# Performance work log

Hardware: AMD Instinct MI355X
Metric: run time of the kernel (lower is better)

## Reference

```python
import jax, jax.numpy as jnp
import numpy as np

B, C, H, W = 8, 384, 32, 32
HEADS = 12


def _relative_position_index(h, w):
    coords_h = np.arange(h)
    coords_w = np.arange(w)
    coords = np.stack(np.meshgrid(coords_h, coords_w, indexing='ij'))  # [2,h,w]
    flat = coords.reshape(2, -1)  # [2, N]
    rel = flat[:, :, None] - flat[:, None, :]  # [2, N, N]
    rel = rel.transpose(1, 2, 0)  # [N, N, 2]
    rel[:, :, 0] += h - 1
    rel[:, :, 1] += w - 1
    rel[:, :, 0] *= 2 * w - 1
    return rel.sum(-1).astype(np.int32)  # [N, N]


def setup_inputs() -> dict:
    key = jax.random.key(0)
    ks = jax.random.split(key, 6)
    std = 0.02
    x = jax.random.normal(ks[0], (B, C, H, W), dtype=jnp.float32)
    q_w = jax.random.normal(ks[1], (C, C), dtype=jnp.float32) * std
    q_b = jnp.zeros((C,), dtype=jnp.float32)
    kv_w = jax.random.normal(ks[2], (2 * C, C), dtype=jnp.float32) * std
    kv_b = jnp.zeros((2 * C,), dtype=jnp.float32)
    proj_w = jax.random.normal(ks[3], (C, C), dtype=jnp.float32) * std
    proj_b = jnp.zeros((C,), dtype=jnp.float32)
    n_table = (2 * H - 1) * (2 * W - 1)
    rpb_table = jax.random.normal(ks[4], (n_table, HEADS), dtype=jnp.float32) * std
    rel_index = jnp.asarray(_relative_position_index(H, W))  # [N, N] int32
    return {"x": x, "q_w": q_w, "q_b": q_b, "kv_w": kv_w, "kv_b": kv_b,
            "proj_w": proj_w, "proj_b": proj_b, "rpb_table": rpb_table,
            "rel_index": rel_index}


def reference(x, q_w, q_b, kv_w, kv_b, proj_w, proj_b, rpb_table, rel_index):
    b, c, h, w = x.shape
    n = h * w
    heads = rpb_table.shape[-1]
    hd = c // heads
    scale = hd ** (-0.5)

    xf = x.reshape(b, c, n)  # 1x1 conv == per-pixel matmul
    q = jnp.einsum('dc,bcn->bdn', q_w, xf) + q_b[:, None]
    q = q.reshape(b, heads, hd, n).transpose(0, 1, 3, 2)  # [b,h,n,hd]
    kv = jnp.einsum('dc,bcn->bdn', kv_w, xf) + kv_b[:, None]
    kv = kv.reshape(b, 2, heads, hd, n)
    k = kv[:, 0].transpose(0, 1, 3, 2)  # [b,h,n,hd]
    v = kv[:, 1].transpose(0, 1, 3, 2)

    attn = jnp.einsum('bhnd,bhmd->bhnm', q, k) * scale  # [b,h,n,n]
    bias = rpb_table[rel_index.reshape(-1)].reshape(n, n, heads)
    bias = bias.transpose(2, 0, 1)  # [h,n,n]
    attn = jax.nn.softmax(attn + bias[None], axis=-1)

    out = jnp.einsum('bhnm,bhmd->bhnd', attn, v)
    out = out.transpose(0, 1, 3, 2).reshape(b, c, h, w)
    out = jnp.einsum('dc,bchw->bdhw', proj_w, out) + proj_b[None, :, None, None]
    return out
```

## Files before the change

### kernel.cpp

```cpp
#include <hip/hip_runtime.h>
#include <hip/hip_bf16.h>

#define B_  8
#define C_  384
#define N_  1024
#define NH_ 12
#define HD_ 32
#define D3_ 1152

typedef __bf16 bf16x8 __attribute__((ext_vector_type(8)));
typedef __bf16 bf16x2 __attribute__((ext_vector_type(2)));
typedef float  f32x4  __attribute__((ext_vector_type(4)));

typedef const __attribute__((address_space(1))) unsigned int guint;
typedef __attribute__((address_space(3))) unsigned int luint;

__device__ __forceinline__ float b2f(ushort u) {
    return __uint_as_float(((unsigned int)u) << 16);
}
__device__ __forceinline__ ushort f2b(float f) {
    unsigned int i = __float_as_uint(f);
    unsigned int r = i + 0x7fffu + ((i >> 16) & 1u);
    return (ushort)(r >> 16);
}
__device__ __forceinline__ unsigned pk2(float a, float b) {
#if __has_builtin(__builtin_amdgcn_cvt_pk_bf16_f32)
    bf16x2 t = __builtin_amdgcn_cvt_pk_bf16_f32(a, b);
    return __builtin_bit_cast(unsigned, t);
#else
    return (unsigned)f2b(a) | ((unsigned)f2b(b) << 16);
#endif
}

#if __has_builtin(__builtin_amdgcn_exp2f)
#define EXP2 __builtin_amdgcn_exp2f
#else
#define EXP2 exp2f
#endif

__device__ __forceinline__ void gl2lds16(const void* g, void* l) {
    __builtin_amdgcn_global_load_lds((guint*)g, (luint*)l, 16, 0, 0);
}

#define C1_ 0.25505654204433796f
#define C2_ 1.4426950408889634f

__global__ __launch_bounds__(256) void setup(
    const float* __restrict__ x, const float* __restrict__ q_w,
    const float* __restrict__ kv_w, const float* __restrict__ proj_w,
    const float* __restrict__ q_b, const float* __restrict__ kv_b,
    const float* __restrict__ tab,
    ushort* __restrict__ xT, float* __restrict__ tabT,
    ushort* __restrict__ Wall, ushort* __restrict__ PW,
    float* __restrict__ ballf)
{
    __shared__ ushort T[64 * 72];
    const int bx = blockIdx.x, tid = threadIdx.x;

    if (bx < 768) {
        int t = bx;
        int nx = t & 15, cy = (t >> 4) % 6, b = t / 96;
        int n0 = nx * 64, c0 = cy * 64;
        {
            int i = tid >> 2;
            int ns = (tid & 3) * 16;
            const float* src = x + ((size_t)b * C_ + c0 + i) * N_ + n0 + ns;
            #pragma unroll
            for (int k4 = 0; k4 < 4; ++k4) {
                float4 f = *(const float4*)(src + k4 * 4);
                T[(ns + k4 * 4 + 0) * 72 + i] = f2b(f.x);
                T[(ns + k4 * 4 + 1) * 72 + i] = f2b(f.y);
                T[(ns + k4 * 4 + 2) * 72 + i] = f2b(f.z);
                T[(ns + k4 * 4 + 3) * 72 + i] = f2b(f.w);
            }
        }
        __syncthreads();
        {
            int j = tid >> 2;
            int cs = (tid & 3) * 16;
            ushort* dst = xT + ((size_t)b * N_ + n0 + j) * C_ + c0 + cs;
            *(uint4*)dst       = *(const uint4*)&T[j * 72 + cs];
            *(uint4*)(dst + 8) = *(const uint4*)&T[j * 72 + cs + 8];
        }
    } else if (bx < 1346) {
        const int NW4 = 110592, NP4 = 36864, NB4 = 288;
        int t = (bx - 768) * 256 + tid;
        if (t < NW4) {
            int e = t * 4;
            float4 f = (e < 147456) ? *(const float4*)(q_w + e)
                                    : *(const float4*)(kv_w + e - 147456);
            union { uint2 u; ushort s[4]; } o;
            o.u.x = pk2(f.x, f.y); o.u.y = pk2(f.z, f.w);
            *(uint2*)(Wall + e) = o.u;
        } else if (t < NW4 + NP4) {
            int e = (t - NW4) * 4;
            float4 f = *(const float4*)(proj_w + e);
            union { uint2 u; ushort s[4]; } o;
            o.u.x = pk2(f.x, f.y); o.u.y = pk2(f.z, f.w);
            *(uint2*)(PW + e) = o.u;
        } else if (t < NW4 + NP4 + NB4) {
            int e = (t - NW4 - NP4) * 4;
            float4 f = (e < 384) ? *(const float4*)(q_b + e)
                                 : *(const float4*)(kv_b + e - 384);
            *(float4*)(ballf + e) = f;
        }
    } else {
        int h = bx - 1346;
        for (int i = tid; i < 3969; i += 256) {
            int dyf = i / 63;
            int src = 3906 + i - 126 * dyf;
            tabT[h * 3969 + i] = tab[(size_t)src * NH_ + h] * C2_;
        }
    }
}

__global__ __launch_bounds__(256) void qkv_gemm4(
    const ushort* __restrict__ xT, const ushort* __restrict__ Wall,
    const float* __restrict__ ballf, ushort* __restrict__ Qt,
    ushort* __restrict__ Kt, ushort* __restrict__ Vtc)
{
    const int b = blockIdx.z, n0 = blockIdx.x * 128, d0 = blockIdx.y * 128;
    __shared__ ushort As[128 * 32];
    __shared__ ushort Bs[128 * 32];
    const int tid = threadIdx.x;
    const int lane = tid & 63, wave = tid >> 6;
    const int quad = lane >> 4, l16 = lane & 15;
    const int wn = (wave & 1) * 64, wd = (wave >> 1) * 64;

    f32x4 acc[4][4] = {};
    const ushort* xb = xT + ((size_t)b * N_ + n0) * C_;
    const ushort* wb = Wall + (size_t)d0 * C_;
    const int rowA = wave * 16 + (lane >> 2);
    const int fstage = ((lane >> 2) ^ (lane >> 4)) & 3;
    const int coff = ((lane & 3) ^ fstage) * 8;
    const int fread = ((l16 & 3) ^ ((l16 >> 2) & 3));

    for (int c0 = 0; c0 < C_; c0 += 32) {
        #pragma unroll
        for (int k = 0; k < 2; ++k) {
            gl2lds16(xb + (size_t)(k * 64 + rowA) * C_ + c0 + coff,
                     &As[(size_t)(k * 256 + wave * 64) * 8]);
            gl2lds16(wb + (size_t)(k * 64 + rowA) * C_ + c0 + coff,
                     &Bs[(size_t)(k * 256 + wave * 64) * 8]);
        }
        __syncthreads();
        bf16x8 af[4], bfr[4];
        #pragma unroll
        for (int i = 0; i < 4; ++i)
            af[i] = *(const bf16x8*)&As[(wn + i * 16 + l16) * 32 + (quad ^ fread) * 8];
        #pragma unroll
        for (int j = 0; j < 4; ++j)
            bfr[j] = *(const bf16x8*)&Bs[(wd + j * 16 + l16) * 32 + (quad ^ fread) * 8];
        #pragma unroll
        for (int i = 0; i < 4; ++i)
            #pragma unroll
            for (int j = 0; j < 4; ++j)
                acc[i][j] = __builtin_amdgcn_mfma_f32_16x16x32_bf16(af[i], bfr[j], acc[i][j], 0, 0, 0);
        __syncthreads();
    }

    if (d0 < 768) {
        ushort* dst = (d0 < 384) ? Qt : Kt;
        const float sc = (d0 < 384) ? C1_ : 1.0f;
        const int hb = ((d0 < 384) ? d0 : d0 - 384) >> 5;
        #pragma unroll
        for (int j = 0; j < 4; ++j) {
            int dloc = wd + j * 16 + l16;
            int h = hb + (dloc >> 5), dc = dloc & 31;
            float bv = ballf[d0 + dloc];
            size_t base = ((size_t)(b * NH_ + h) * N_) * 32 + dc;
            #pragma unroll
            for (int i = 0; i < 4; ++i) {
                int nbase = n0 + wn + i * 16 + quad * 4;
                #pragma unroll
                for (int r = 0; r < 4; ++r)
                    dst[base + (size_t)(nbase + r) * 32] = f2b((acc[i][j][r] + bv) * sc);
            }
        }
    } else {
        #pragma unroll
        for (int j = 0; j < 4; ++j) {
            int dloc = wd + j * 16 + l16;
            int vd = d0 - 768 + dloc;
            int h = vd >> 5, dc = vd & 31;
            float bv = ballf[d0 + dloc];
            size_t hbase = (size_t)(b * NH_ + h) * 32768 + dc * 32;
            #pragma unroll
            for (int i = 0; i < 4; ++i) {
                int n = n0 + wn + i * 16 + quad * 4;
                size_t cbase = hbase + (size_t)((n >> 5)) * 1024 + (n & 31);
                uint2 w;
                w.x = pk2(acc[i][j][0] + bv, acc[i][j][1] + bv);
                w.y = pk2(acc[i][j][2] + bv, acc[i][j][3] + bv);
                *(uint2*)(Vtc + cbase) = w;
            }
        }
    }
}

__global__ __launch_bounds__(256) void attn4(
    const ushort* __restrict__ Qt, const ushort* __restrict__ Kt,
    const ushort* __restrict__ Vtc, const float* __restrict__ tabT,
    ushort* __restrict__ O)
{
    const int bid = blockIdx.x;
    const int bh96 = bid % 96;
    const int nx = bid / 96;
    const int b = bh96 / 12, h = bh96 % 12;

    __shared__ float tabL[3972];
    __shared__ ushort Pa[8192];

    const int tid = threadIdx.x;
    const int lane = tid & 63, wave = tid >> 6;
    const int quad = lane >> 4, l16 = lane & 15;
    const int bh = b * NH_ + h;

    {
        const float* th = tabT + h * 3969;
        for (int i = tid; i < 3969; i += 256) tabL[i] = th[i];
    }
    __syncthreads();

    const int qs0 = nx * 8 + wave * 2;
    const ushort* Kbh = Kt + (size_t)bh * N_ * 32;
    const ushort* Vbh = Vtc + (size_t)bh * 16 * 2048;

    bf16x8 qf[2];
    int ib[2];
    #pragma unroll
    for (int st = 0; st < 2; ++st) {
        int q = (qs0 + st) * 16 + l16;
        qf[st] = *(const bf16x8*)(Qt + ((size_t)bh * N_ + q) * 32 + quad * 8);
        int qy = q >> 5, qx = q & 31;
        ib[st] = (31 - qy) * 63 + qx + 31;
    }

    int off_tr[16];
    #pragma unroll
    for (int t = 0; t < 4; ++t)
        #pragma unroll
        for (int r = 0; r < 4; ++r) {
            int ml = t * 16 + quad * 4 + r;
            off_tr[t * 4 + r] = (ml >> 5) * 63 - (ml & 31);
        }

    f32x4 oacc[2][2] = {};
    float rs[2] = {0.f, 0.f};

    ushort* PwBase = &Pa[wave * 2048];
    const int pswz = l16 & 0xE;

    for (int mc = 0; mc < 16; ++mc) {
        const ushort* kp = Kbh + mc * 64 * 32;
        bf16x8 k0 = *(const bf16x8*)(kp + (0 * 16 + l16) * 32 + quad * 8);
        bf16x8 k1 = *(const bf16x8*)(kp + (1 * 16 + l16) * 32 + quad * 8);
        bf16x8 k2 = *(const bf16x8*)(kp + (2 * 16 + l16) * 32 + quad * 8);
        bf16x8 k3 = *(const bf16x8*)(kp + (3 * 16 + l16) * 32 + quad * 8);
        const ushort* vp = Vbh + mc * 2048;
        bf16x8 va[2][2];
        #pragma unroll
        for (int kc = 0; kc < 2; ++kc)
            #pragma unroll
            for (int dt = 0; dt < 2; ++dt)
                va[kc][dt] = *(const bf16x8*)(vp + kc * 1024 + (dt * 16 + l16) * 32 + quad * 8);

        #pragma unroll
        for (int st = 0; st < 2; ++st) {
            const int ibm = ib[st] + mc * 126;
            f32x4 cb[4];
            #pragma unroll
            for (int t = 0; t < 4; ++t) {
                cb[t][0] = tabL[ibm + off_tr[t * 4 + 0]];
                cb[t][1] = tabL[ibm + off_tr[t * 4 + 1]];
                cb[t][2] = tabL[ibm + off_tr[t * 4 + 2]];
                cb[t][3] = tabL[ibm + off_tr[t * 4 + 3]];
            }
            f32x4 s0 = __builtin_amdgcn_mfma_f32_16x16x32_bf16(k0, qf[st], cb[0], 0, 0, 0);
            f32x4 s1 = __builtin_amdgcn_mfma_f32_16x16x32_bf16(k1, qf[st], cb[1], 0, 0, 0);
            f32x4 s2 = __builtin_amdgcn_mfma_f32_16x16x32_bf16(k2, qf[st], cb[2], 0, 0, 0);
            f32x4 s3 = __builtin_amdgcn_mfma_f32_16x16x32_bf16(k3, qf[st], cb[3], 0, 0, 0);

            ushort* Pw = PwBase + st * 1024;
            f32x4 sv[4] = {s0, s1, s2, s3};
            #pragma unroll
            for (int t = 0; t < 4; ++t) {
                float p0 = EXP2(sv[t][0]);
                float p1 = EXP2(sv[t][1]);
                float p2 = EXP2(sv[t][2]);
                float p3 = EXP2(sv[t][3]);
                rs[st] += (p0 + p1) + (p2 + p3);
                uint2 w;
                w.x = pk2(p0, p1);
                w.y = pk2(p2, p3);
                *(uint2*)(Pw + l16 * 64 + (((t * 4 + quad) ^ pswz) * 4)) = w;
            }
            #pragma unroll
            for (int kc = 0; kc < 2; ++kc) {
                bf16x8 pb = *(const bf16x8*)(Pw + l16 * 64 + (((kc * 8 + quad * 2) ^ pswz) * 4));
                oacc[st][0] = __builtin_amdgcn_mfma_f32_16x16x32_bf16(va[kc][0], pb, oacc[st][0], 0, 0, 0);
                oacc[st][1] = __builtin_amdgcn_mfma_f32_16x16x32_bf16(va[kc][1], pb, oacc[st][1], 0, 0, 0);
            }
        }
    }

    #pragma unroll
    for (int st = 0; st < 2; ++st) {
        float s = rs[st];
        s += __shfl_xor(s, 16, 64);
        s += __shfl_xor(s, 32, 64);
        rs[st] = 1.0f / s;
    }

    #pragma unroll
    for (int st = 0; st < 2; ++st) {
        int q = (qs0 + st) * 16 + l16;
        ushort* ob = O + ((size_t)(b * N_ + q)) * C_ + h * HD_;
        #pragma unroll
        for (int dt = 0; dt < 2; ++dt) {
            uint2 w;
            w.x = pk2(oacc[st][dt][0] * rs[st], oacc[st][dt][1] * rs[st]);
            w.y = pk2(oacc[st][dt][2] * rs[st], oacc[st][dt][3] * rs[st]);
            *(uint2*)(ob + dt * 16 + quad * 4) = w;
        }
    }
}

__global__ __launch_bounds__(256) void proj_gemm3(
    const ushort* __restrict__ O, const ushort* __restrict__ PW,
    const float* __restrict__ pb, float* __restrict__ out)
{
    const int b = blockIdx.z, n0 = blockIdx.x * 128, d0 = blockIdx.y * 128;
    __shared__ ushort As[128 * 32];
    __shared__ ushort Bs[128 * 32];
    const int tid = threadIdx.x;
    const int lane = tid & 63, wave = tid >> 6;
    const int quad = lane >> 4, l16 = lane & 15;
    const int wa = (wave & 1) * 64, wb = (wave >> 1) * 64;

    f32x4 acc[4][4] = {};
    const ushort* ab = PW + (size_t)d0 * C_;
    const ushort* bbp = O + ((size_t)b * N_ + n0) * C_;
    const int rowA = wave * 16 + (lane >> 2);
    const int fstage = ((lane >> 2) ^ (lane >> 4)) & 3;
    const int coff = ((lane & 3) ^ fstage) * 8;
    const int fread = ((l16 & 3) ^ ((l16 >> 2) & 3));

    for (int c0 = 0; c0 < C_; c0 += 32) {
        #pragma unroll
        for (int k = 0; k < 2; ++k) {
            gl2lds16(ab + (size_t)(k * 64 + rowA) * C_ + c0 + coff,
                     &As[(size_t)(k * 256 + wave * 64) * 8]);
            gl2lds16(bbp + (size_t)(k * 64 + rowA) * C_ + c0 + coff,
                     &Bs[(size_t)(k * 256 + wave * 64) * 8]);
        }
        __syncthreads();
        bf16x8 af[4], bfr[4];
        #pragma unroll
        for (int i = 0; i < 4; ++i)
            af[i] = *(const bf16x8*)&As[(wa + i * 16 + l16) * 32 + (quad ^ fread) * 8];
        #pragma unroll
        for (int j = 0; j < 4; ++j)
            bfr[j] = *(const bf16x8*)&Bs[(wb + j * 16 + l16) * 32 + (quad ^ fread) * 8];
        #pragma unroll
        for (int i = 0; i < 4; ++i)
            #pragma unroll
            for (int j = 0; j < 4; ++j)
                acc[i][j] = __builtin_amdgcn_mfma_f32_16x16x32_bf16(af[i], bfr[j], acc[i][j], 0, 0, 0);
        __syncthreads();
    }

    #pragma unroll
    for (int i = 0; i < 4; ++i) {
        #pragma unroll
        for (int r = 0; r < 4; ++r) {
            int d = d0 + wa + i * 16 + quad * 4 + r;
            float bv = pb[d];
            float* op = out + ((size_t)b * C_ + d) * N_ + n0 + wb;
            #pragma unroll
            for (int j = 0; j < 4; ++j)
                op[j * 16 + l16] = acc[i][j][r] + bv;
        }
    }
}

extern "C" void kernel_launch(void* const* d_in, const int* in_sizes, int n_in,
                              void* d_out, int out_size, void* d_ws, size_t ws_size,
                              hipStream_t stream)
{
    const float* x      = (const float*)d_in[0];
    const float* q_w    = (const float*)d_in[1];
    const float* q_b    = (const float*)d_in[2];
    const float* kv_w   = (const float*)d_in[3];
    const float* kv_b   = (const float*)d_in[4];
    const float* proj_w = (const float*)d_in[5];
    const float* proj_b = (const float*)d_in[6];
    const float* rpb    = (const float*)d_in[7];
    float* out = (float*)d_out;

    char* ws = (char*)d_ws;
    ushort* xT    = (ushort*)(ws);
    ushort* Qt    = (ushort*)(ws +  6291456);
    ushort* Kt    = (ushort*)(ws + 12582912);
    ushort* Vtc   = (ushort*)(ws + 18874368);
    ushort* O     = (ushort*)(ws + 25165824);
    float*  tabT  = (float*) (ws + 31457280);
    ushort* Wall  = (ushort*)(ws + 31647808);
    ushort* PW    = (ushort*)(ws + 32532544);
    float*  ballf = (float*) (ws + 32827456);

    setup      <<<dim3(1358), 256, 0, stream>>>(x, q_w, kv_w, proj_w, q_b, kv_b, rpb,
                                                xT, tabT, Wall, PW, ballf);
    qkv_gemm4  <<<dim3(8, 9, B_), 256, 0, stream>>>(xT, Wall, ballf, Qt, Kt, Vtc);
    attn4      <<<dim3(768), 256, 0, stream>>>(Qt, Kt, Vtc, tabT, O);
    proj_gemm3 <<<dim3(8, 3, B_), 256, 0, stream>>>(O, PW, proj_b, out);
}
```

Before: 152.5 us.

## Reverse bias table layout for contiguous loads and vectorize QK stores

Stores the relative-position bias table reversed and padded, so each lane's four bias values per MFMA tile sit contiguously. Six vector loads per key chunk are then shared across both query subtiles instead of sixteen scattered scalar LDS reads per subtile. The Q/K GEMM swaps MFMA operand order so the epilogue can write packed 4-element bf16 stores instead of scalar strided stores. The bias table is copied to LDS with float4 loads. This shifts workspace offsets and relies on the index algebra holding for the fixed 32x32 geometry.

```diff
diff --git a/kernel.cpp b/kernel.cpp
--- a/kernel.cpp
+++ b/kernel.cpp
@@ -44,6 +44,7 @@
 
 #define C1_ 0.25505654204433796f
 #define C2_ 1.4426950408889634f
+#define TS_ 3972
 
 __global__ __launch_bounds__(256) void setup(
     const float* __restrict__ x, const float* __restrict__ q_w,
@@ -106,15 +107,13 @@
         }
     } else {
         int h = bx - 1346;
-        for (int i = tid; i < 3969; i += 256) {
-            int dyf = i / 63;
-            int src = 3906 + i - 126 * dyf;
-            tabT[h * 3969 + i] = tab[(size_t)src * NH_ + h] * C2_;
-        }
-    }
-}
-
-__global__ __launch_bounds__(256) void qkv_gemm4(
+        for (int i = tid; i < 3969; i += 256)
+            tabT[h * TS_ + i] = tab[(size_t)(3968 - i) * NH_ + h] * C2_;
+        if (tid < 3) tabT[h * TS_ + 3969 + tid] = 0.0f;
+    }
+}
+
+__global__ __launch_bounds__(256) void qkv_gemm5(
     const ushort* __restrict__ xT, const ushort* __restrict__ Wall,
     const float* __restrict__ ballf, ushort* __restrict__ Qt,
     ushort* __restrict__ Kt, ushort* __restrict__ Vtc)
@@ -134,6 +133,7 @@
     const int fstage = ((lane >> 2) ^ (lane >> 4)) & 3;
     const int coff = ((lane & 3) ^ fstage) * 8;
     const int fread = ((l16 & 3) ^ ((l16 >> 2) & 3));
+    const bool isV = (d0 >= 768);
 
     for (int c0 = 0; c0 < C_; c0 += 32) {
         #pragma unroll
@@ -151,30 +151,41 @@
         #pragma unroll
         for (int j = 0; j < 4; ++j)
             bfr[j] = *(const bf16x8*)&Bs[(wd + j * 16 + l16) * 32 + (quad ^ fread) * 8];
-        #pragma unroll
-        for (int i = 0; i < 4; ++i)
-            #pragma unroll
-            for (int j = 0; j < 4; ++j)
-                acc[i][j] = __builtin_amdgcn_mfma_f32_16x16x32_bf16(af[i], bfr[j], acc[i][j], 0, 0, 0);
+        if (!isV) {
+            #pragma unroll
+            for (int i = 0; i < 4; ++i)
+                #pragma unroll
+                for (int j = 0; j < 4; ++j)
+                    acc[i][j] = __builtin_amdgcn_mfma_f32_16x16x32_bf16(bfr[i], af[j], acc[i][j], 0, 0, 0);
+        } else {
+            #pragma unroll
+            for (int i = 0; i < 4; ++i)
+                #pragma unroll
+                for (int j = 0; j < 4; ++j)
+                    acc[i][j] = __builtin_amdgcn_mfma_f32_16x16x32_bf16(af[i], bfr[j], acc[i][j], 0, 0, 0);
+        }
         __syncthreads();
     }
 
-    if (d0 < 768) {
+    if (!isV) {
         ushort* dst = (d0 < 384) ? Qt : Kt;
         const float sc = (d0 < 384) ? C1_ : 1.0f;
-        const int hb = ((d0 < 384) ? d0 : d0 - 384) >> 5;
-        #pragma unroll
-        for (int j = 0; j < 4; ++j) {
-            int dloc = wd + j * 16 + l16;
-            int h = hb + (dloc >> 5), dc = dloc & 31;
-            float bv = ballf[d0 + dloc];
-            size_t base = ((size_t)(b * NH_ + h) * N_) * 32 + dc;
-            #pragma unroll
-            for (int i = 0; i < 4; ++i) {
-                int nbase = n0 + wn + i * 16 + quad * 4;
-                #pragma unroll
-                for (int r = 0; r < 4; ++r)
-                    dst[base + (size_t)(nbase + r) * 32] = f2b((acc[i][j][r] + bv) * sc);
+        const int reg0 = (d0 < 384) ? 0 : 384;
+        #pragma unroll
+        for (int i = 0; i < 4; ++i) {
+            int dloc = wd + i * 16;
+            int dg = d0 - reg0 + dloc;
+            int h = dg >> 5;
+            int dc = (dg & 31) + quad * 4;
+            float4 bvv = *(const float4*)(ballf + d0 + dloc + quad * 4);
+            size_t hb = (size_t)(b * NH_ + h) * N_;
+            #pragma unroll
+            for (int j = 0; j < 4; ++j) {
+                int n = n0 + wn + j * 16 + l16;
+                uint2 w;
+                w.x = pk2((acc[i][j][0] + bvv.x) * sc, (acc[i][j][1] + bvv.y) * sc);
+                w.y = pk2((acc[i][j][2] + bvv.z) * sc, (acc[i][j][3] + bvv.w) * sc);
+                *(uint2*)(dst + (hb + n) * 32 + dc) = w;
             }
         }
     } else {
@@ -198,7 +209,7 @@
     }
 }
 
-__global__ __launch_bounds__(256) void attn4(
+__global__ __launch_bounds__(256) void attn5(
     const ushort* __restrict__ Qt, const ushort* __restrict__ Kt,
     const ushort* __restrict__ Vtc, const float* __restrict__ tabT,
     ushort* __restrict__ O)
@@ -208,7 +219,7 @@
     const int nx = bid / 96;
     const int b = bh96 / 12, h = bh96 % 12;
 
-    __shared__ float tabL[3972];
+    __shared__ float tabL[TS_];
     __shared__ ushort Pa[8192];
 
     const int tid = threadIdx.x;
@@ -217,8 +228,13 @@
     const int bh = b * NH_ + h;
 
     {
-        const float* th = tabT + h * 3969;
-        for (int i = tid; i < 3969; i += 256) tabL[i] = th[i];
+        const float* th = tabT + h * TS_;
+        int i = tid * 4;
+        #pragma unroll
+        for (int k = 0; k < 4; ++k) {
+            if (i < TS_) *(float4*)&tabL[i] = *(const float4*)&th[i];
+            i += 1024;
+        }
     }
     __syncthreads();
 
@@ -227,23 +243,16 @@
     const ushort* Vbh = Vtc + (size_t)bh * 16 * 2048;
 
     bf16x8 qf[2];
-    int ib[2];
     #pragma unroll
     for (int st = 0; st < 2; ++st) {
         int q = (qs0 + st) * 16 + l16;
         qf[st] = *(const bf16x8*)(Qt + ((size_t)bh * N_ + q) * 32 + quad * 8);
-        int qy = q >> 5, qx = q & 31;
-        ib[st] = (31 - qy) * 63 + qx + 31;
-    }
-
-    int off_tr[16];
-    #pragma unroll
-    for (int t = 0; t < 4; ++t)
-        #pragma unroll
-        for (int r = 0; r < 4; ++r) {
-            int ml = t * 16 + quad * 4 + r;
-            off_tr[t * 4 + r] = (ml >> 5) * 63 - (ml & 31);
-        }
+    }
+    int ibx0;
+    {
+        int q = qs0 * 16 + l16;
+        ibx0 = (31 - (q >> 5)) * 63 + (31 - (q & 31));
+    }
 
     f32x4 oacc[2][2] = {};
     float rs[2] = {0.f, 0.f};
@@ -265,21 +274,25 @@
             for (int dt = 0; dt < 2; ++dt)
                 va[kc][dt] = *(const bf16x8*)(vp + kc * 1024 + (dt * 16 + l16) * 32 + quad * 8);
 
+        const float* Tb = tabL + ibx0 + mc * 126 + quad * 4;
+        f32x4 tvm16, tv0, tv16, tv47, tv63, tv79;
+        #pragma unroll
+        for (int e = 0; e < 4; ++e) {
+            tvm16[e] = Tb[e - 16];
+            tv0[e]   = Tb[e];
+            tv16[e]  = Tb[e + 16];
+            tv47[e]  = Tb[e + 47];
+            tv63[e]  = Tb[e + 63];
+            tv79[e]  = Tb[e + 79];
+        }
+        f32x4 cbs[2][4] = {{tv0, tv16, tv63, tv79}, {tvm16, tv0, tv47, tv63}};
+
         #pragma unroll
         for (int st = 0; st < 2; ++st) {
-            const int ibm = ib[st] + mc * 126;
-            f32x4 cb[4];
-            #pragma unroll
-            for (int t = 0; t < 4; ++t) {
-                cb[t][0] = tabL[ibm + off_tr[t * 4 + 0]];
-                cb[t][1] = tabL[ibm + off_tr[t * 4 + 1]];
-                cb[t][2] = tabL[ibm + off_tr[t * 4 + 2]];
-                cb[t][3] = tabL[ibm + off_tr[t * 4 + 3]];
-            }
-            f32x4 s0 = __builtin_amdgcn_mfma_f32_16x16x32_bf16(k0, qf[st], cb[0], 0, 0, 0);
-            f32x4 s1 = __builtin_amdgcn_mfma_f32_16x16x32_bf16(k1, qf[st], cb[1], 0, 0, 0);
-            f32x4 s2 = __builtin_amdgcn_mfma_f32_16x16x32_bf16(k2, qf[st], cb[2], 0, 0, 0);
-            f32x4 s3 = __builtin_amdgcn_mfma_f32_16x16x32_bf16(k3, qf[st], cb[3], 0, 0, 0);
+            f32x4 s0 = __builtin_amdgcn_mfma_f32_16x16x32_bf16(k0, qf[st], cbs[st][0], 0, 0, 0);
+            f32x4 s1 = __builtin_amdgcn_mfma_f32_16x16x32_bf16(k1, qf[st], cbs[st][1], 0, 0, 0);
+            f32x4 s2 = __builtin_amdgcn_mfma_f32_16x16x32_bf16(k2, qf[st], cbs[st][2], 0, 0, 0);
+            f32x4 s3 = __builtin_amdgcn_mfma_f32_16x16x32_bf16(k3, qf[st], cbs[st][3], 0, 0, 0);
 
             ushort* Pw = PwBase + st * 1024;
             f32x4 sv[4] = {s0, s1, s2, s3};
@@ -405,13 +418,13 @@
     ushort* Vtc   = (ushort*)(ws + 18874368);
     ushort* O     = (ushort*)(ws + 25165824);
     float*  tabT  = (float*) (ws + 31457280);
-    ushort* Wall  = (ushort*)(ws + 31647808);
-    ushort* PW    = (ushort*)(ws + 32532544);
-    float*  ballf = (float*) (ws + 32827456);
+    ushort* Wall  = (ushort*)(ws + 31647936);
+    ushort* PW    = (ushort*)(ws + 32532672);
+    float*  ballf = (float*) (ws + 32827584);
 
     setup      <<<dim3(1358), 256, 0, stream>>>(x, q_w, kv_w, proj_w, q_b, kv_b, rpb,
                                                 xT, tabT, Wall, PW, ballf);
-    qkv_gemm4  <<<dim3(8, 9, B_), 256, 0, stream>>>(xT, Wall, ballf, Qt, Kt, Vtc);
-    attn4      <<<dim3(768), 256, 0, stream>>>(Qt, Kt, Vtc, tabT, O);
+    qkv_gemm5  <<<dim3(8, 9, B_), 256, 0, stream>>>(xT, Wall, ballf, Qt, Kt, Vtc);
+    attn5      <<<dim3(768), 256, 0, stream>>>(Qt, Kt, Vtc, tabT, O);
     proj_gemm3 <<<dim3(8, 3, B_), 256, 0, stream>>>(O, PW, proj_b, out);
 }
```

Measured after the change: 150.9 us. About the same (-1.1%).
